# Optimization experiments

Measured on AMD Instinct MI355X. Metric: run time of the kernel, lower is better.

Reference implementation:

```python
import jax, jax.numpy as jnp
import numpy as np


def setup_inputs() -> dict:
    key = jax.random.key(0)
    k1, k2, k3, k4 = jax.random.split(key, 4)
    num_tokens, hidden = 16384, 7168
    head_dim, coff = 512, 1            # compress_ratio=128 -> coff=1
    compress_ratio = 128
    num_blocks, block_size = 4096, 8   # block_size=8 for compress_ratio=128
    x = jax.random.normal(k1, (num_tokens, hidden), jnp.float32) * 0.02
    W = jax.random.normal(k2, (2 * coff * head_dim, hidden), jnp.float32) * 0.02
    ape = jax.random.normal(k3, (compress_ratio, coff * head_dim), jnp.float32)
    state_cache = jnp.zeros((num_blocks, block_size, 2 * coff * head_dim), jnp.float32)
    positions = jax.random.randint(k4, (num_tokens,), 0, 131072, dtype=jnp.int32)
    slot_mapping = jnp.arange(num_tokens, dtype=jnp.int32)  # unique, in-range slots
    return {"x": x, "W": W, "ape": ape, "state_cache": state_cache,
            "positions": positions, "slot_mapping": slot_mapping, "block_size": 8}


def reference(x, W, ape, state_cache, positions, slot_mapping, block_size):
    # fused_wkv_wgate GEMM (cublas bf16->fp32 in original): [T,H] @ [H,2D] -> [T,2D]
    kv_score = jnp.einsum('th,dh->td', x, W)
    D = W.shape[0] // 2                      # coff * head_dim (state_width)
    kv, score = kv_score[:, :D], kv_score[:, D:]
    compress_ratio = ape.shape[0]
    # fused APE lookup: ape[position % COMPRESS_RATIO] added to score half
    ape_rows = ape[positions % compress_ratio]          # [T, D]
    new_vals = jnp.concatenate([kv, score + ape_rows], axis=-1)  # [T, 2D]
    num_blocks, bs, width = state_cache.shape
    # slot -> (block_idx, pos_in_block) is exactly flat indexing for a
    # contiguous [num_blocks, block_size, width] cache.
    flat = state_cache.reshape(num_blocks * bs, width)
    # slot < 0 tokens are skipped (mapped out of range + mode='drop')
    idx = jnp.where(slot_mapping >= 0, slot_mapping, num_blocks * bs)
    flat = flat.at[idx].set(new_vals, mode='drop')
    return flat.reshape(num_blocks, bs, width)
```

## Files before the change

kernel.cpp:

```cpp
#include <hip/hip_runtime.h>
#include <hip/hip_bf16.h>
#include <stdint.h>


typedef short  bf16x8 __attribute__((ext_vector_type(8)));
typedef float  f32x4  __attribute__((ext_vector_type(4)));

#define BM 128
#define BN 128
#define BK 32
#define NT 256

__device__ __forceinline__ uint32_t pack_bf16x2(float lo, float hi) {
    uint32_t a = __float_as_uint(lo);
    uint32_t b = __float_as_uint(hi);
    a += 0x7fffu + ((a >> 16) & 1u);
    b += 0x7fffu + ((b >> 16) & 1u);
    return (a >> 16) | (b & 0xffff0000u);
}

__device__ __forceinline__ void gload_lds16(const uint16_t* g, uint16_t* l) {
    __builtin_amdgcn_global_load_lds(
        (const __attribute__((address_space(1))) uint32_t*)g,
        (__attribute__((address_space(3))) uint32_t*)l,
        16, 0, 0);
}

__global__ void set_flags(const int* __restrict__ slots, uint8_t* __restrict__ flags,
                          int num_tokens, int num_slots) {
    const int i = blockIdx.x * blockDim.x + threadIdx.x;
    if (i < num_tokens) {
        const int s = slots[i];
        if (s >= 0 && s < num_slots) flags[s] = 1;
    }
}

__global__ void prep(const float4* __restrict__ cache, float4* __restrict__ out,
                     const uint8_t* __restrict__ flags,
                     const float4* __restrict__ x, uint4* __restrict__ xb,
                     const float4* __restrict__ w, uint4* __restrict__ wb,
                     int n_c4, int nx8, int nw8) {
    const int i = blockIdx.x * blockDim.x + threadIdx.x;
    if (i < n_c4) {
        if (!flags[i >> 8]) out[i] = cache[i];
    } else if (i < n_c4 + nx8) {
        const int j = i - n_c4;
        const float4 a = x[2 * j];
        const float4 b = x[2 * j + 1];
        uint4 o;
        o.x = pack_bf16x2(a.x, a.y);
        o.y = pack_bf16x2(a.z, a.w);
        o.z = pack_bf16x2(b.x, b.y);
        o.w = pack_bf16x2(b.z, b.w);
        xb[j] = o;
    } else if (i < n_c4 + nx8 + nw8) {
        const int j = i - n_c4 - nx8;
        const float4 a = w[2 * j];
        const float4 b = w[2 * j + 1];
        uint4 o;
        o.x = pack_bf16x2(a.x, a.y);
        o.y = pack_bf16x2(a.z, a.w);
        o.z = pack_bf16x2(b.x, b.y);
        o.w = pack_bf16x2(b.z, b.w);
        wb[j] = o;
    }
}

__global__ __launch_bounds__(NT, 4)
void gemm_bf16_scatter(const uint16_t* __restrict__ XB, const uint16_t* __restrict__ WB,
                       const float* __restrict__ ape, const int* __restrict__ positions,
                       const int* __restrict__ slots, float* __restrict__ out,
                       int K, int D, int CR, int num_slots, int n_tiles_m)
{
    __shared__ uint16_t ldsA[BM * BK];
    __shared__ uint16_t ldsB[BN * BK];

    const int tile_m = blockIdx.x % n_tiles_m;
    const int tile_n = blockIdx.x / n_tiles_m;
    const int t    = threadIdx.x;
    const int lane = t & 63;
    const int wid  = t >> 6;
    const int wm   = (wid >> 1) * 64;
    const int wn   = (wid & 1) * 64;
    const int fr   = lane & 15;
    const int fc   = lane >> 4;
    const int swz  = (fc ^ ((fr >> 1) & 3)) << 3;

    const int p0 = t, p1 = t + NT;
    const int r0 = p0 >> 2, c0 = (p0 & 3) ^ ((r0 >> 1) & 3);
    const int r1 = p1 >> 2, c1 = (p1 & 3) ^ ((r1 >> 1) & 3);

    const uint16_t* gA0 = XB + (size_t)(tile_m * BM + r0) * K + c0 * 8;
    const uint16_t* gA1 = XB + (size_t)(tile_m * BM + r1) * K + c1 * 8;
    const uint16_t* gB0 = WB + (size_t)(tile_n * BN + r0) * K + c0 * 8;
    const uint16_t* gB1 = WB + (size_t)(tile_n * BN + r1) * K + c1 * 8;
    uint16_t* lA0 = &ldsA[p0 * 8];
    uint16_t* lA1 = &ldsA[p1 * 8];
    uint16_t* lB0 = &ldsB[p0 * 8];
    uint16_t* lB1 = &ldsB[p1 * 8];

    f32x4 acc[4][4];
    #pragma unroll
    for (int i = 0; i < 4; i++)
        #pragma unroll
        for (int j = 0; j < 4; j++)
            acc[i][j] = f32x4{0.f, 0.f, 0.f, 0.f};

    for (int k0 = 0; k0 < K; k0 += BK) {
        gload_lds16(gA0 + k0, lA0);
        gload_lds16(gA1 + k0, lA1);
        gload_lds16(gB0 + k0, lB0);
        gload_lds16(gB1 + k0, lB1);
        __syncthreads();

        bf16x8 af[4], bfrag[4];
        #pragma unroll
        for (int i = 0; i < 4; i++)
            af[i] = *(const bf16x8*)&ldsA[(wm + i * 16 + fr) * BK + swz];
        #pragma unroll
        for (int j = 0; j < 4; j++)
            bfrag[j] = *(const bf16x8*)&ldsB[(wn + j * 16 + fr) * BK + swz];

        #pragma unroll
        for (int i = 0; i < 4; i++)
            #pragma unroll
            for (int j = 0; j < 4; j++)
                acc[i][j] = __builtin_amdgcn_mfma_f32_16x16x32_bf16(af[i], bfrag[j], acc[i][j], 0, 0, 0);
        __syncthreads();
    }

    const int D2 = 2 * D;
    #pragma unroll
    for (int i = 0; i < 4; i++) {
        #pragma unroll
        for (int r = 0; r < 4; r++) {
            const int token = tile_m * BM + wm + i * 16 + fc * 4 + r;
            const int slot  = slots[token];
            if (slot < 0 || slot >= num_slots) continue;
            const int p = positions[token] % CR;
            const float* aperow = ape + (size_t)p * D;
            float* orow = out + (size_t)slot * D2;
            #pragma unroll
            for (int j = 0; j < 4; j++) {
                const int col = tile_n * BN + wn + j * 16 + fr;
                float v = acc[i][j][r];
                if (col >= D) v += aperow[col - D];
                orow[col] = v;
            }
        }
    }
}

__global__ void copy_cache(const float4* __restrict__ src, float4* __restrict__ dst, int n4) {
    const int i = blockIdx.x * blockDim.x + threadIdx.x;
    if (i < n4) dst[i] = src[i];
}

__device__ __forceinline__ int lds_idx_f(int row, int chunk) {
    return row * BK + ((chunk ^ ((row >> 1) & 3)) << 3);
}

__global__ __launch_bounds__(NT, 2)
void gemm_scatter_f32(const float* __restrict__ X, const float* __restrict__ Wm,
                      const float* __restrict__ ape, const int* __restrict__ positions,
                      const int* __restrict__ slots, float* __restrict__ out,
                      int K, int D, int CR, int num_slots, int n_tiles_n)
{
    __shared__ uint16_t ldsA[BM * BK];
    __shared__ uint16_t ldsB[BN * BK];

    const int tile_m = blockIdx.x / n_tiles_n;
    const int tile_n = blockIdx.x % n_tiles_n;
    const int t    = threadIdx.x;
    const int lane = t & 63;
    const int wid  = t >> 6;
    const int wm   = (wid >> 1) * 64;
    const int wn   = (wid & 1) * 64;
    const int fr   = lane & 15;
    const int fc   = lane >> 4;
    const int swz  = fc ^ ((fr >> 1) & 3);

    const float* Abase = X  + (size_t)(tile_m * BM) * K;
    const float* Bbase = Wm + (size_t)(tile_n * BN) * K;

    f32x4 acc[4][4];
    #pragma unroll
    for (int i = 0; i < 4; i++)
        #pragma unroll
        for (int j = 0; j < 4; j++)
            acc[i][j] = f32x4{0.f, 0.f, 0.f, 0.f};

    for (int k0 = 0; k0 < K; k0 += BK) {
        #pragma unroll
        for (int i = 0; i < 4; i++) {
            const int lin = t + i * NT;
            const int row = lin >> 3;
            const int c4  = lin & 7;
            const int half = c4 & 1;
            const int sidx = lds_idx_f(row, c4 >> 1) + half * 4;

            const float4 va = *(const float4*)(Abase + (size_t)row * K + k0 + c4 * 4);
            uint2 pa; pa.x = pack_bf16x2(va.x, va.y); pa.y = pack_bf16x2(va.z, va.w);
            *(uint2*)&ldsA[sidx] = pa;

            const float4 vb = *(const float4*)(Bbase + (size_t)row * K + k0 + c4 * 4);
            uint2 pb; pb.x = pack_bf16x2(vb.x, vb.y); pb.y = pack_bf16x2(vb.z, vb.w);
            *(uint2*)&ldsB[sidx] = pb;
        }
        __syncthreads();

        bf16x8 af[4], bfrag[4];
        #pragma unroll
        for (int i = 0; i < 4; i++)
            af[i] = *(const bf16x8*)&ldsA[(wm + i * 16 + fr) * BK + (swz << 3)];
        #pragma unroll
        for (int j = 0; j < 4; j++)
            bfrag[j] = *(const bf16x8*)&ldsB[(wn + j * 16 + fr) * BK + (swz << 3)];

        #pragma unroll
        for (int i = 0; i < 4; i++)
            #pragma unroll
            for (int j = 0; j < 4; j++)
                acc[i][j] = __builtin_amdgcn_mfma_f32_16x16x32_bf16(af[i], bfrag[j], acc[i][j], 0, 0, 0);
        __syncthreads();
    }

    const int D2 = 2 * D;
    #pragma unroll
    for (int i = 0; i < 4; i++) {
        #pragma unroll
        for (int r = 0; r < 4; r++) {
            const int token = tile_m * BM + wm + i * 16 + fc * 4 + r;
            const int slot  = slots[token];
            if (slot < 0 || slot >= num_slots) continue;
            const int p = positions[token] % CR;
            const float* aperow = ape + (size_t)p * D;
            float* orow = out + (size_t)slot * D2;
            #pragma unroll
            for (int j = 0; j < 4; j++) {
                const int col = tile_n * BN + wn + j * 16 + fr;
                float v = acc[i][j][r];
                if (col >= D) v += aperow[col - D];
                orow[col] = v;
            }
        }
    }
}

extern "C" void kernel_launch(void* const* d_in, const int* in_sizes, int n_in,
                              void* d_out, int out_size, void* d_ws, size_t ws_size,
                              hipStream_t stream) {
    const float* x         = (const float*)d_in[0];
    const float* W         = (const float*)d_in[1];
    const float* ape       = (const float*)d_in[2];
    const float* cache     = (const float*)d_in[3];
    const int*   positions = (const int*)d_in[4];
    const int*   slots     = (const int*)d_in[5];
    float* out = (float*)d_out;

    const int num_tokens = in_sizes[4];
    const int hidden     = in_sizes[0] / num_tokens;
    const int D2         = in_sizes[1] / hidden;
    const int D          = D2 / 2;
    const int CR         = in_sizes[2] / D;
    const int num_slots  = in_sizes[3] / D2;

    const int n_tiles_m = num_tokens / BM;
    const int n_tiles_n = D2 / BN;

    const size_t nx = (size_t)in_sizes[0];
    const size_t nw = (size_t)in_sizes[1];
    const size_t need = (nx + nw) * sizeof(uint16_t) + (size_t)num_slots;

    if (ws_size >= need) {
        uint16_t* xb = (uint16_t*)d_ws;
        uint16_t* wb = xb + nx;
        uint8_t* flags = (uint8_t*)(wb + nw);

        hipMemsetAsync(flags, 0, num_slots, stream);
        set_flags<<<(num_tokens + 255) / 256, 256, 0, stream>>>(slots, flags, num_tokens, num_slots);

        const int n_c4 = out_size / 4;
        const int nx8  = (int)(nx / 8);
        const int nw8  = (int)(nw / 8);
        const int total = n_c4 + nx8 + nw8;
        prep<<<(total + 255) / 256, 256, 0, stream>>>(
            (const float4*)cache, (float4*)out, flags,
            (const float4*)x, (uint4*)xb, (const float4*)W, (uint4*)wb,
            n_c4, nx8, nw8);

        gemm_bf16_scatter<<<n_tiles_m * n_tiles_n, NT, 0, stream>>>(
            xb, wb, ape, positions, slots, out, hidden, D, CR, num_slots, n_tiles_m);
    } else {
        const int n4 = out_size / 4;
        copy_cache<<<(n4 + 255) / 256, 256, 0, stream>>>((const float4*)cache, (float4*)out, n4);
        gemm_scatter_f32<<<n_tiles_m * n_tiles_n, NT, 0, stream>>>(
            x, W, ape, positions, slots, out, hidden, D, CR, num_slots, n_tiles_n);
    }
}
```

Before: 1.060 ms.

## Add 256x256x64 double-buffered bf16 MFMA GEMM with XOR-swizzled LDS

```diff
diff --git a/kernel.cpp b/kernel.cpp
--- a/kernel.cpp
+++ b/kernel.cpp
@@ -10,6 +10,11 @@
 #define BN 128
 #define BK 32
 #define NT 256
+
+#define GBM 256
+#define GBN 256
+#define GBK 64
+#define GNT 512
 
 __device__ __forceinline__ uint32_t pack_bf16x2(float lo, float hi) {
     uint32_t a = __float_as_uint(lo);
@@ -66,6 +71,134 @@
     }
 }
 
+__global__ __launch_bounds__(GNT, 2)
+void gemm_bf16_scatter_256(const uint16_t* __restrict__ XB, const uint16_t* __restrict__ WB,
+                           const float* __restrict__ ape, const int* __restrict__ positions,
+                           const int* __restrict__ slots, float* __restrict__ out,
+                           int K, int D, int CR, int num_slots, int n_tiles_m, int n_tiles_n)
+{
+    __shared__ uint16_t lds[2 * 2 * GBM * GBK];
+
+    const int t    = threadIdx.x;
+    const int lane = t & 63;
+    const int wid  = t >> 6;
+    const int wr   = wid >> 2;
+    const int wc   = wid & 3;
+    const int fr   = lane & 15;
+    const int fc4  = lane >> 4;
+
+    const int nblk = n_tiles_m * n_tiles_n;
+    int tidx = blockIdx.x;
+    if ((nblk & 7) == 0) {
+        const int per = nblk >> 3;
+        tidx = (tidx & 7) * per + (tidx >> 3);
+    }
+    const int tile_m = tidx / n_tiles_n;
+    const int tile_n = tidx % n_tiles_n;
+
+    const int rr = t >> 3;
+    const int cs = ((t & 7) ^ (rr & 7)) * 8;
+    const uint16_t* gA = XB + (size_t)(tile_m * GBM + rr) * K + cs;
+    const uint16_t* gB = WB + (size_t)(tile_n * GBN + rr) * K + cs;
+    uint16_t* const dst0 = lds + t * 8;
+
+    const int c0 = (fc4 ^ (fr & 7)) * 8;
+    const int c1 = ((4 + fc4) ^ (fr & 7)) * 8;
+    const int arow0 = (wr * 128 + fr) * GBK;
+    const int brow0 = (wc * 64 + fr) * GBK;
+
+    f32x4 acc[8][4];
+    #pragma unroll
+    for (int i = 0; i < 8; i++)
+        #pragma unroll
+        for (int j = 0; j < 4; j++)
+            acc[i][j] = f32x4{0.f, 0.f, 0.f, 0.f};
+
+    const int nkt = K / GBK;
+
+#define STAGE256(cur_, kt_) do {                                            \
+    uint16_t* dA_ = dst0 + (cur_) * (2 * GBM * GBK);                        \
+    uint16_t* dB_ = dA_ + (GBM * GBK);                                      \
+    const size_t ko_ = (size_t)(kt_) * GBK;                                 \
+    _Pragma("unroll")                                                       \
+    for (int q_ = 0; q_ < 4; q_++) {                                        \
+        gload_lds16(gA + ko_ + (size_t)q_ * 64 * K, dA_ + q_ * 4096);       \
+        gload_lds16(gB + ko_ + (size_t)q_ * 64 * K, dB_ + q_ * 4096);       \
+    }                                                                       \
+} while (0)
+
+    STAGE256(0, 0);
+    if (nkt > 1) STAGE256(1, 1);
+
+    for (int kt = 0; kt < nkt; ++kt) {
+        const int cur = kt & 1;
+        if (kt + 1 < nkt) asm volatile("s_waitcnt vmcnt(8)" ::: "memory");
+        else              asm volatile("s_waitcnt vmcnt(0)" ::: "memory");
+        __builtin_amdgcn_s_barrier();
+        asm volatile("" ::: "memory");
+        __builtin_amdgcn_sched_barrier(0);
+
+        const uint16_t* A = lds + cur * (2 * GBM * GBK);
+        const uint16_t* B = A + GBM * GBK;
+
+        #pragma unroll
+        for (int h = 0; h < 2; ++h) {
+            const int cN = h ? c1 : c0;
+            bf16x8 bfr[4];
+            #pragma unroll
+            for (int j = 0; j < 4; ++j)
+                bfr[j] = *(const bf16x8*)(B + brow0 + j * (16 * GBK) + cN);
+            #pragma unroll
+            for (int mh = 0; mh < 2; ++mh) {
+                bf16x8 afr[4];
+                #pragma unroll
+                for (int i = 0; i < 4; ++i)
+                    afr[i] = *(const bf16x8*)(A + arow0 + mh * (64 * GBK) + i * (16 * GBK) + cN);
+                __builtin_amdgcn_s_setprio(1);
+                #pragma unroll
+                for (int i = 0; i < 4; ++i)
+                    #pragma unroll
+                    for (int j = 0; j < 4; ++j)
+                        acc[mh * 4 + i][j] = __builtin_amdgcn_mfma_f32_16x16x32_bf16(
+                            afr[i], bfr[j], acc[mh * 4 + i][j], 0, 0, 0);
+                __builtin_amdgcn_s_setprio(0);
+            }
+        }
+
+        __builtin_amdgcn_sched_barrier(0);
+        asm volatile("" ::: "memory");
+        __builtin_amdgcn_s_barrier();
+        asm volatile("" ::: "memory");
+        __builtin_amdgcn_sched_barrier(0);
+        if (kt + 2 < nkt) STAGE256(cur, kt + 2);
+    }
+#undef STAGE256
+
+    const int D2 = 2 * D;
+    const int mbase = tile_m * GBM + wr * 128 + fc4 * 4;
+    const int nbase = tile_n * GBN + wc * 64 + fr;
+    #pragma unroll
+    for (int ai = 0; ai < 8; ++ai) {
+        #pragma unroll
+        for (int r = 0; r < 4; ++r) {
+            const int token = mbase + ai * 16 + r;
+            const int slot  = slots[token];
+            if (slot < 0 || slot >= num_slots) continue;
+            int p = positions[token];
+            p = (CR & (CR - 1)) ? (p % CR) : (p & (CR - 1));
+            const float* aperow = ape + (size_t)p * D;
+            float* orow = out + (size_t)slot * D2;
+            #pragma unroll
+            for (int j = 0; j < 4; ++j) {
+                const int col = nbase + j * 16;
+                float v = acc[ai][j][r];
+                if (col >= D) v += aperow[col - D];
+                orow[col] = v;
+            }
+        }
+    }
+}
+
 __global__ __launch_bounds__(NT, 4)
 void gemm_bf16_scatter(const uint16_t* __restrict__ XB, const uint16_t* __restrict__ WB,
                        const float* __restrict__ ape, const int* __restrict__ positions,
@@ -289,8 +422,17 @@
             (const float4*)x, (uint4*)xb, (const float4*)W, (uint4*)wb,
             n_c4, nx8, nw8);
 
-        gemm_bf16_scatter<<<n_tiles_m * n_tiles_n, NT, 0, stream>>>(
-            xb, wb, ape, positions, slots, out, hidden, D, CR, num_slots, n_tiles_m);
+        const bool div256 = (num_tokens % GBM == 0) && (D2 % GBN == 0) &&
+                            (hidden % GBK == 0) && (hidden / GBK >= 1);
+        if (div256) {
+            const int tm = num_tokens / GBM;
+            const int tn = D2 / GBN;
+            gemm_bf16_scatter_256<<<tm * tn, GNT, 0, stream>>>(
+                xb, wb, ape, positions, slots, out, hidden, D, CR, num_slots, tm, tn);
+        } else {
+            gemm_bf16_scatter<<<n_tiles_m * n_tiles_n, NT, 0, stream>>>(
+                xb, wb, ape, positions, slots, out, hidden, D, CR, num_slots, n_tiles_m);
+        }
     } else {
         const int n4 = out_size / 4;
         copy_cache<<<(n4 + 255) / 256, 256, 0, stream>>>((const float4*)cache, (float4*)out, n4);
```

Result: faster. 997.4 us (-5.9%).
